# Kernel tuning notes

Hardware: AMD Instinct MI355X
Metric: run time of the kernel (lower is better)

Reference implementation:

```python
import jax, jax.numpy as jnp
import numpy as np

B, S, D = 1, 4096, 1024
H, G = 16, 4
DK = D // H            # 64, per-head dim
HKV = H // G           # 4 KV heads
DKV = D // G           # 256, KV projection width
SCALE = 1.0 / np.sqrt(np.float32(DK))


def setup_inputs() -> dict:
    key = jax.random.key(0)
    ks = jax.random.split(key, 10)
    std = 0.02
    return {
        "x": jax.random.normal(ks[0], (B, S, D), jnp.float32),
        "mask": jax.random.bernoulli(ks[1], 0.1, (B, 1, S)),  # True = masked out
        "Wq": jax.random.normal(ks[2], (D, D), jnp.float32) * std,
        "bq": jnp.zeros((D,), jnp.float32),
        "Wk": jax.random.normal(ks[3], (D, DKV), jnp.float32) * std,
        "bk": jnp.zeros((DKV,), jnp.float32),
        "Wv": jax.random.normal(ks[4], (D, DKV), jnp.float32) * std,
        "bv": jnp.zeros((DKV,), jnp.float32),
        "Wo": jax.random.normal(ks[5], (D, D), jnp.float32) * std,
        "bo": jnp.zeros((D,), jnp.float32),
    }


def reference(x, mask, Wq, bq, Wk, bk, Wv, bv, Wo, bo):
    b, s, _ = x.shape
    # projections
    q = (x @ Wq + bq).reshape(b, s, H, DK).transpose(0, 2, 1, 3)      # [B,H,S,DK]
    k = (x @ Wk + bk).reshape(b, s, HKV, DK).transpose(0, 2, 1, 3)    # [B,HKV,S,DK]
    v = (x @ Wv + bv).reshape(b, s, HKV, DK).transpose(0, 2, 1, 3)    # [B,HKV,S,DK]
    # expand KV heads: head h = kv_head * G + g (matches torch expand+reshape)
    k = jnp.repeat(k, G, axis=1)                                       # [B,H,S,DK]
    v = jnp.repeat(v, G, axis=1)                                       # [B,H,S,DK]
    scores = jnp.einsum("bhsd,bhtd->bhst", q, k) * SCALE              # [B,H,S,S]
    neg_inf = jnp.finfo(scores.dtype).min
    scores = jnp.where(mask[:, None, :, :], neg_inf, scores)           # mask: [B,1,1,S]
    attn = jax.nn.softmax(scores, axis=-1)
    out = jnp.einsum("bhst,bhtd->bhsd", attn, v)                      # [B,H,S,DK]
    out = out.transpose(0, 2, 1, 3).reshape(b, s, D)
    return out @ Wo + bo
```

## Files before the change

kernel.cpp:

```cpp
#include <hip/hip_runtime.h>
#include <cstdint>
#include <cstddef>

#define S_LEN 4096
#define DMODEL 1024
#define NHEADS 16
#define HDK 64
#define DKV 256
#define NTOT 1536
#define QSCALE 0.18033688011112042f

typedef __bf16 bf16;
typedef __bf16 bf16x8 __attribute__((ext_vector_type(8)));
typedef float f32x4 __attribute__((ext_vector_type(4)));

typedef __attribute__((address_space(3))) void lds_void;
typedef const __attribute__((address_space(1))) void gbl_void;

__device__ __forceinline__ void gload16(const void* g, void* l) {
  __builtin_amdgcn_global_load_lds((gbl_void*)g, (lds_void*)l, 16, 0, 0);
}

__global__ __launch_bounds__(256) void prep(
    const float* __restrict__ x, const int* __restrict__ mask,
    const float* __restrict__ Wq, const float* __restrict__ Wk,
    const float* __restrict__ Wv, const float* __restrict__ Wo,
    bf16* __restrict__ xb, float* __restrict__ mkf, bf16* __restrict__ mkb,
    bf16* __restrict__ Wqt, bf16* __restrict__ Wkt,
    bf16* __restrict__ Wvt, bf16* __restrict__ Wot) {
  const int z = blockIdx.z;
  if (z < 4) {
    const float* src;
    bf16* dst;
    int C;
    switch (z) {
      case 0: src = Wq; dst = Wqt; C = DMODEL; break;
      case 1: src = Wk; dst = Wkt; C = DKV; break;
      case 2: src = Wv; dst = Wvt; C = DKV; break;
      default: src = Wo; dst = Wot; C = DMODEL; break;
    }
    const int c0 = blockIdx.x * 32;
    if (c0 >= C) return;
    __shared__ float tile[32][33];
    const int tx = threadIdx.x & 31;
    const int ty = threadIdx.x >> 5;
    const int r0 = blockIdx.y * 32;
#pragma unroll
    for (int i = 0; i < 4; i++)
      tile[ty + i * 8][tx] = src[(size_t)(r0 + ty + i * 8) * C + c0 + tx];
    __syncthreads();
#pragma unroll
    for (int i = 0; i < 4; i++)
      dst[(size_t)(c0 + ty + i * 8) * DMODEL + r0 + tx] = (bf16)tile[tx][ty + i * 8];
  } else {
    const int b = blockIdx.y * 32 + blockIdx.x;
    const int half = z - 4;
    const int i = ((half * 1024 + b) * 256 + (int)threadIdx.x) * 8;
    float4 a = *(const float4*)(x + i);
    float4 c = *(const float4*)(x + i + 4);
    bf16 o[8] = {(bf16)a.x, (bf16)a.y, (bf16)a.z, (bf16)a.w,
                 (bf16)c.x, (bf16)c.y, (bf16)c.z, (bf16)c.w};
    *(uint4*)(xb + i) = *(uint4*)o;
    if (half == 1 && b < 2) {
      const int mi = (b * 256 + (int)threadIdx.x) * 8;
#pragma unroll
      for (int j = 0; j < 8; j++) {
        float keep = mask[mi + j] ? 0.0f : 1.0f;
        mkf[mi + j] = keep;
        mkb[mi + j] = (bf16)keep;
      }
    }
  }
}

template <int QKV>
__global__ __launch_bounds__(256) void gemm_ld(
    const bf16* __restrict__ A, const bf16* __restrict__ Bt, int M, int N, int K,
    const float* __restrict__ bq, const float* __restrict__ bk,
    const float* __restrict__ bv, const float* __restrict__ mkf,
    bf16* __restrict__ Qb, bf16* __restrict__ Kb, bf16* __restrict__ Vtb,
    const float* __restrict__ bo, float* __restrict__ Co) {
  __shared__ bf16 As[128 * 64];
  __shared__ bf16 Bs[128 * 64];
  const int t = threadIdx.x;
  const int lane = t & 63;
  const int wave = t >> 6;
  const int m0 = blockIdx.y * 128;
  const int n0 = blockIdx.x * 128;
  const int wm = (wave >> 1) * 64;
  const int wn = (wave & 1) * 64;
  const int lr = lane & 15;
  const int quad = lane >> 4;

  const int sr = lane >> 3;
  const int sc = ((lane & 7) ^ (lane >> 3)) * 8;

  f32x4 acc[4][4] = {};

  for (int k0 = 0; k0 < K; k0 += 64) {
    __syncthreads();
#pragma unroll
    for (int j = 0; j < 4; j++) {
      const int rbase = wave * 32 + j * 8;
      gload16(A + (size_t)(m0 + rbase + sr) * K + k0 + sc, &As[rbase * 64]);
      gload16(Bt + (size_t)(n0 + rbase + sr) * K + k0 + sc, &Bs[rbase * 64]);
    }
    __syncthreads();
#pragma unroll
    for (int kh2 = 0; kh2 < 2; kh2++) {
      const int fo = ((kh2 * 4 + quad) ^ (lr & 7)) * 8;
      bf16x8 af[4], bfr[4];
#pragma unroll
      for (int mt = 0; mt < 4; mt++)
        af[mt] = *(const bf16x8*)(&As[(wm + mt * 16 + lr) * 64 + fo]);
#pragma unroll
      for (int nt = 0; nt < 4; nt++)
        bfr[nt] = *(const bf16x8*)(&Bs[(wn + nt * 16 + lr) * 64 + fo]);
#pragma unroll
      for (int mt = 0; mt < 4; mt++)
#pragma unroll
        for (int nt = 0; nt < 4; nt++)
          acc[mt][nt] = __builtin_amdgcn_mfma_f32_16x16x32_bf16(af[mt], bfr[nt], acc[mt][nt], 0, 0, 0);
    }
  }

#pragma unroll
  for (int nt = 0; nt < 4; nt++) {
    const int n = n0 + wn + nt * 16 + lr;
    if (QKV) {
      if (n < DMODEL) {
        const float b = bq[n];
#pragma unroll
        for (int mt = 0; mt < 4; mt++)
#pragma unroll
          for (int r = 0; r < 4; r++) {
            const int m = m0 + wm + mt * 16 + quad * 4 + r;
            Qb[(size_t)m * DMODEL + n] = (bf16)((acc[mt][nt][r] + b) * QSCALE);
          }
      } else if (n < DMODEL + DKV) {
        const float b = bk[n - DMODEL];
#pragma unroll
        for (int mt = 0; mt < 4; mt++)
#pragma unroll
          for (int r = 0; r < 4; r++) {
            const int m = m0 + wm + mt * 16 + quad * 4 + r;
            Kb[(size_t)m * DKV + (n - DMODEL)] = (bf16)(acc[mt][nt][r] + b);
          }
      } else {
        const float b = bv[n - DMODEL - DKV];
#pragma unroll
        for (int mt = 0; mt < 4; mt++)
#pragma unroll
          for (int r = 0; r < 4; r++) {
            const int m = m0 + wm + mt * 16 + quad * 4 + r;
            Vtb[(size_t)(n - DMODEL - DKV) * S_LEN + m] = (bf16)((acc[mt][nt][r] + b) * mkf[m]);
          }
      }
    } else {
      const float b = bo[n];
#pragma unroll
      for (int mt = 0; mt < 4; mt++)
#pragma unroll
        for (int r = 0; r < 4; r++) {
          const int m = m0 + wm + mt * 16 + quad * 4 + r;
          Co[(size_t)m * N + n] = acc[mt][nt][r] + b;
        }
    }
  }
}

__global__ __launch_bounds__(256) void flash_attn(
    const bf16* __restrict__ Q, const bf16* __restrict__ K,
    const bf16* __restrict__ Vt, const bf16* __restrict__ mkb,
    bf16* __restrict__ O) {
  const int h = blockIdx.y;
  const int kvh = h >> 2;
  const int q0 = blockIdx.x * 128;
  const int t = threadIdx.x;
  const int lane = t & 63;
  const int wave = t >> 6;
  const int lr = lane & 15;
  const int quad = lane >> 4;

  __shared__ bf16 Ks[128][72];
  __shared__ bf16 Vs[64][136];
  __shared__ bf16 Ps[4][32][36];
  __shared__ bf16 mks[128];

  bf16x8 aq[2][2];
#pragma unroll
  for (int qt = 0; qt < 2; qt++) {
    const int qrow = q0 + wave * 32 + qt * 16 + lr;
    aq[qt][0] = *(const bf16x8*)(Q + (size_t)qrow * DMODEL + h * HDK + quad * 8);
    aq[qt][1] = *(const bf16x8*)(Q + (size_t)qrow * DMODEL + h * HDK + 32 + quad * 8);
  }

  f32x4 o_acc[2][4] = {};
  f32x4 l_acc[2] = {};

  for (int kv0 = 0; kv0 < S_LEN; kv0 += 128) {
    __syncthreads();
#pragma unroll
    for (int i = 0; i < 4; i++) {
      int id = t + i * 256;
      int row = id >> 3;
      int ch = (id & 7) * 8;
      uint4 d = *(const uint4*)(K + (size_t)(kv0 + row) * DKV + kvh * HDK + ch);
      *(uint4*)(&Ks[row][ch]) = d;
    }
#pragma unroll
    for (int i = 0; i < 4; i++) {
      int id = t + i * 256;
      int row = id >> 4;
      int ch = (id & 15) * 8;
      uint4 d = *(const uint4*)(Vt + (size_t)(kvh * HDK + row) * S_LEN + kv0 + ch);
      *(uint4*)(&Vs[row][ch]) = d;
    }
    if (t < 16) *(uint4*)(&mks[t * 8]) = *(const uint4*)(mkb + kv0 + t * 8);
    __syncthreads();

#pragma unroll
    for (int kc = 0; kc < 4; kc++) {
      bf16x8 ak[2][2];
#pragma unroll
      for (int ntl = 0; ntl < 2; ntl++) {
        const int krow = kc * 32 + ntl * 16 + lr;
        ak[ntl][0] = *(const bf16x8*)(&Ks[krow][quad * 8]);
        ak[ntl][1] = *(const bf16x8*)(&Ks[krow][32 + quad * 8]);
      }
#pragma unroll
      for (int qt = 0; qt < 2; qt++) {
#pragma unroll
        for (int ntl = 0; ntl < 2; ntl++) {
          f32x4 s = {};
          s = __builtin_amdgcn_mfma_f32_16x16x32_bf16(ak[ntl][0], aq[qt][0], s, 0, 0, 0);
          s = __builtin_amdgcn_mfma_f32_16x16x32_bf16(ak[ntl][1], aq[qt][1], s, 0, 0, 0);
          bf16 p4[4];
#pragma unroll
          for (int r = 0; r < 4; r++) p4[r] = (bf16)__builtin_amdgcn_exp2f(s[r]);
          *(uint2*)(&Ps[wave][qt * 16 + lr][ntl * 16 + quad * 4]) = *(uint2*)p4;
        }
      }
      bf16x8 bvf[4];
#pragma unroll
      for (int ntv = 0; ntv < 4; ntv++)
        bvf[ntv] = *(const bf16x8*)(&Vs[ntv * 16 + lr][kc * 32 + quad * 8]);
      bf16x8 mkfv = *(const bf16x8*)(&mks[kc * 32 + quad * 8]);
#pragma unroll
      for (int qt = 0; qt < 2; qt++) {
        bf16x8 ap = *(const bf16x8*)(&Ps[wave][qt * 16 + lr][quad * 8]);
#pragma unroll
        for (int ntv = 0; ntv < 4; ntv++)
          o_acc[qt][ntv] = __builtin_amdgcn_mfma_f32_16x16x32_bf16(ap, bvf[ntv], o_acc[qt][ntv], 0, 0, 0);
        l_acc[qt] = __builtin_amdgcn_mfma_f32_16x16x32_bf16(ap, mkfv, l_acc[qt], 0, 0, 0);
      }
    }
  }

#pragma unroll
  for (int qt = 0; qt < 2; qt++) {
#pragma unroll
    for (int ntv = 0; ntv < 4; ntv++) {
#pragma unroll
      for (int r = 0; r < 4; r++) {
        const int row = q0 + wave * 32 + qt * 16 + quad * 4 + r;
        O[(size_t)row * DMODEL + h * HDK + ntv * 16 + lr] =
            (bf16)(o_acc[qt][ntv][r] / l_acc[qt][r]);
      }
    }
  }
}

extern "C" void kernel_launch(void* const* d_in, const int* in_sizes, int n_in,
                              void* d_out, int out_size, void* d_ws, size_t ws_size,
                              hipStream_t stream) {
  const float* x = (const float*)d_in[0];
  const int* mask = (const int*)d_in[1];
  const float* Wq = (const float*)d_in[2];
  const float* bq = (const float*)d_in[3];
  const float* Wk = (const float*)d_in[4];
  const float* bk = (const float*)d_in[5];
  const float* Wv = (const float*)d_in[6];
  const float* bv = (const float*)d_in[7];
  const float* Wo = (const float*)d_in[8];
  const float* bo = (const float*)d_in[9];
  float* out = (float*)d_out;

  char* w = (char*)d_ws;
  bf16* xb  = (bf16*)w; w += (size_t)S_LEN * DMODEL * 2;
  bf16* Wqt = (bf16*)w; w += (size_t)DMODEL * DMODEL * 2;
  bf16* Wkt = (bf16*)w; w += (size_t)DKV * DMODEL * 2;
  bf16* Wvt = (bf16*)w; w += (size_t)DKV * DMODEL * 2;
  bf16* Wot = (bf16*)w; w += (size_t)DMODEL * DMODEL * 2;
  bf16* Qb  = (bf16*)w; w += (size_t)S_LEN * DMODEL * 2;
  bf16* Kb  = (bf16*)w; w += (size_t)S_LEN * DKV * 2;
  bf16* Vtb = (bf16*)w; w += (size_t)DKV * S_LEN * 2;
  bf16* Ob  = (bf16*)w; w += (size_t)S_LEN * DMODEL * 2;
  float* mkf = (float*)w; w += (size_t)S_LEN * 4;
  bf16* mkb = (bf16*)w; w += (size_t)S_LEN * 2;

  prep<<<dim3(32, 32, 6), 256, 0, stream>>>(
      x, mask, Wq, Wk, Wv, Wo, xb, mkf, mkb, Wqt, Wkt, Wvt, Wot);

  gemm_ld<1><<<dim3(NTOT / 128, S_LEN / 128), 256, 0, stream>>>(
      xb, Wqt, S_LEN, NTOT, DMODEL, bq, bk, bv, mkf, Qb, Kb, Vtb, nullptr, nullptr);

  flash_attn<<<dim3(S_LEN / 128, NHEADS), 256, 0, stream>>>(Qb, Kb, Vtb, mkb, Ob);

  gemm_ld<0><<<dim3(DMODEL / 128, S_LEN / 128), 256, 0, stream>>>(
      Ob, Wot, S_LEN, DMODEL, DMODEL, nullptr, nullptr, nullptr, nullptr,
      nullptr, nullptr, nullptr, bo, out);
}
```

Baseline: 233.6 us.

## Halve GEMM M-tile and register-prefetch next K/V tile in flash attention

The GEMM kernels now use 64x128 tiles instead of 128x128, doubling the grid so more workgroups fill the CUs for these modest-sized projections, at the cost of more B-tile reloads per output. The flash attention kernel now loads the next K, V and mask tile into registers while the current tile is being computed, hiding global load latency behind MFMA work. This raises register pressure in the attention kernel, which may reduce occupancy.

After: 298.5 us. 1.28x slower.

```diff
diff --git a/kernel.cpp b/kernel.cpp
--- a/kernel.cpp
+++ b/kernel.cpp
@@ -80,14 +80,14 @@
     const float* __restrict__ bv, const float* __restrict__ mkf,
     bf16* __restrict__ Qb, bf16* __restrict__ Kb, bf16* __restrict__ Vtb,
     const float* __restrict__ bo, float* __restrict__ Co) {
-  __shared__ bf16 As[128 * 64];
+  __shared__ bf16 As[64 * 64];
   __shared__ bf16 Bs[128 * 64];
   const int t = threadIdx.x;
   const int lane = t & 63;
   const int wave = t >> 6;
-  const int m0 = blockIdx.y * 128;
+  const int m0 = blockIdx.y * 64;
   const int n0 = blockIdx.x * 128;
-  const int wm = (wave >> 1) * 64;
+  const int wm = (wave >> 1) * 32;
   const int wn = (wave & 1) * 64;
   const int lr = lane & 15;
   const int quad = lane >> 4;
@@ -95,29 +95,33 @@
   const int sr = lane >> 3;
   const int sc = ((lane & 7) ^ (lane >> 3)) * 8;
 
-  f32x4 acc[4][4] = {};
+  f32x4 acc[2][4] = {};
 
   for (int k0 = 0; k0 < K; k0 += 64) {
     __syncthreads();
+#pragma unroll
+    for (int j = 0; j < 2; j++) {
+      const int rbase = wave * 16 + j * 8;
+      gload16(A + (size_t)(m0 + rbase + sr) * K + k0 + sc, &As[rbase * 64]);
+    }
 #pragma unroll
     for (int j = 0; j < 4; j++) {
       const int rbase = wave * 32 + j * 8;
-      gload16(A + (size_t)(m0 + rbase + sr) * K + k0 + sc, &As[rbase * 64]);
       gload16(Bt + (size_t)(n0 + rbase + sr) * K + k0 + sc, &Bs[rbase * 64]);
     }
     __syncthreads();
 #pragma unroll
     for (int kh2 = 0; kh2 < 2; kh2++) {
       const int fo = ((kh2 * 4 + quad) ^ (lr & 7)) * 8;
-      bf16x8 af[4], bfr[4];
-#pragma unroll
-      for (int mt = 0; mt < 4; mt++)
+      bf16x8 af[2], bfr[4];
+#pragma unroll
+      for (int mt = 0; mt < 2; mt++)
         af[mt] = *(const bf16x8*)(&As[(wm + mt * 16 + lr) * 64 + fo]);
 #pragma unroll
       for (int nt = 0; nt < 4; nt++)
         bfr[nt] = *(const bf16x8*)(&Bs[(wn + nt * 16 + lr) * 64 + fo]);
 #pragma unroll
-      for (int mt = 0; mt < 4; mt++)
+      for (int mt = 0; mt < 2; mt++)
 #pragma unroll
         for (int nt = 0; nt < 4; nt++)
           acc[mt][nt] = __builtin_amdgcn_mfma_f32_16x16x32_bf16(af[mt], bfr[nt], acc[mt][nt], 0, 0, 0);
@@ -131,7 +135,7 @@
       if (n < DMODEL) {
         const float b = bq[n];
 #pragma unroll
-        for (int mt = 0; mt < 4; mt++)
+        for (int mt = 0; mt < 2; mt++)
 #pragma unroll
           for (int r = 0; r < 4; r++) {
             const int m = m0 + wm + mt * 16 + quad * 4 + r;
@@ -140,7 +144,7 @@
       } else if (n < DMODEL + DKV) {
         const float b = bk[n - DMODEL];
 #pragma unroll
-        for (int mt = 0; mt < 4; mt++)
+        for (int mt = 0; mt < 2; mt++)
 #pragma unroll
           for (int r = 0; r < 4; r++) {
             const int m = m0 + wm + mt * 16 + quad * 4 + r;
@@ -149,7 +153,7 @@
       } else {
         const float b = bv[n - DMODEL - DKV];
 #pragma unroll
-        for (int mt = 0; mt < 4; mt++)
+        for (int mt = 0; mt < 2; mt++)
 #pragma unroll
           for (int r = 0; r < 4; r++) {
             const int m = m0 + wm + mt * 16 + quad * 4 + r;
@@ -159,7 +163,7 @@
     } else {
       const float b = bo[n];
 #pragma unroll
-      for (int mt = 0; mt < 4; mt++)
+      for (int mt = 0; mt < 2; mt++)
 #pragma unroll
         for (int r = 0; r < 4; r++) {
           const int m = m0 + wm + mt * 16 + quad * 4 + r;
@@ -195,6 +199,24 @@
     aq[qt][1] = *(const bf16x8*)(Q + (size_t)qrow * DMODEL + h * HDK + 32 + quad * 8);
   }
 
+  const bf16* Kbase = K + kvh * HDK;
+  const bf16* Vbase = Vt + (size_t)kvh * HDK * S_LEN;
+  int rowK[4], chK[4], rowV[4], chV[4];
+#pragma unroll
+  for (int i = 0; i < 4; i++) {
+    const int id = t + i * 256;
+    rowK[i] = id >> 3;  chK[i] = (id & 7) * 8;
+    rowV[i] = id >> 4;  chV[i] = (id & 15) * 8;
+  }
+
+  uint4 rK[4], rV[4], rM;
+#pragma unroll
+  for (int i = 0; i < 4; i++) {
+    rK[i] = *(const uint4*)(Kbase + (size_t)rowK[i] * DKV + chK[i]);
+    rV[i] = *(const uint4*)(Vbase + (size_t)rowV[i] * S_LEN + chV[i]);
+  }
+  if (t < 16) rM = *(const uint4*)(mkb + t * 8);
+
   f32x4 o_acc[2][4] = {};
   f32x4 l_acc[2] = {};
 
@@ -202,22 +224,21 @@
     __syncthreads();
 #pragma unroll
     for (int i = 0; i < 4; i++) {
-      int id = t + i * 256;
-      int row = id >> 3;
-      int ch = (id & 7) * 8;
-      uint4 d = *(const uint4*)(K + (size_t)(kv0 + row) * DKV + kvh * HDK + ch);
-      *(uint4*)(&Ks[row][ch]) = d;
-    }
-#pragma unroll
-    for (int i = 0; i < 4; i++) {
-      int id = t + i * 256;
-      int row = id >> 4;
-      int ch = (id & 15) * 8;
-      uint4 d = *(const uint4*)(Vt + (size_t)(kvh * HDK + row) * S_LEN + kv0 + ch);
-      *(uint4*)(&Vs[row][ch]) = d;
-    }
-    if (t < 16) *(uint4*)(&mks[t * 8]) = *(const uint4*)(mkb + kv0 + t * 8);
-    __syncthreads();
+      *(uint4*)(&Ks[rowK[i]][chK[i]]) = rK[i];
+      *(uint4*)(&Vs[rowV[i]][chV[i]]) = rV[i];
+    }
+    if (t < 16) *(uint4*)(&mks[t * 8]) = rM;
+    __syncthreads();
+
+    const int kvn = kv0 + 128;
+    if (kvn < S_LEN) {
+#pragma unroll
+      for (int i = 0; i < 4; i++) {
+        rK[i] = *(const uint4*)(Kbase + (size_t)(kvn + rowK[i]) * DKV + chK[i]);
+        rV[i] = *(const uint4*)(Vbase + (size_t)rowV[i] * S_LEN + kvn + chV[i]);
+      }
+      if (t < 16) rM = *(const uint4*)(mkb + kvn + t * 8);
+    }
 
 #pragma unroll
     for (int kc = 0; kc < 4; kc++) {
@@ -302,12 +323,12 @@
   prep<<<dim3(32, 32, 6), 256, 0, stream>>>(
       x, mask, Wq, Wk, Wv, Wo, xb, mkf, mkb, Wqt, Wkt, Wvt, Wot);
 
-  gemm_ld<1><<<dim3(NTOT / 128, S_LEN / 128), 256, 0, stream>>>(
+  gemm_ld<1><<<dim3(NTOT / 128, S_LEN / 64), 256, 0, stream>>>(
       xb, Wqt, S_LEN, NTOT, DMODEL, bq, bk, bv, mkf, Qb, Kb, Vtb, nullptr, nullptr);
 
   flash_attn<<<dim3(S_LEN / 128, NHEADS), 256, 0, stream>>>(Qb, Kb, Vtb, mkb, Ob);
 
-  gemm_ld<0><<<dim3(DMODEL / 128, S_LEN / 128), 256, 0, stream>>>(
+  gemm_ld<0><<<dim3(DMODEL / 128, S_LEN / 64), 256, 0, stream>>>(
       Ob, Wot, S_LEN, DMODEL, DMODEL, nullptr, nullptr, nullptr, nullptr,
       nullptr, nullptr, nullptr, bo, out);
 }
```
